# Optimization experiments

Hardware: AMD Instinct MI355X
Metric: run time of the kernel (lower is better)

Reference implementation:

```python
import jax, jax.numpy as jnp
import numpy as np

DT = 1.0          # integration timestep (ms)
SIGMA = 0.5       # gauss_std for surrogate (unused in pure fwd spike)
AMPLITUDE = 0.3   # dampening_factor
N = 50000         # neurons
R = 4             # receptor types
D = 5             # max_delay
E = 5000000       # recurrent synapses
B = 4             # batch


def setup_inputs() -> dict:
    key = jax.random.key(0)
    ks = jax.random.split(key, 20)
    f = jnp.float32
    inputs = jax.random.normal(ks[0], (B, N * R), f) * 0.1
    # z_buf holds binary spikes for the last D steps
    z_buf = jax.random.bernoulli(ks[1], 0.05, (B, N * D)).astype(f)
    v = jax.random.uniform(ks[2], (B, N), f, 0.0, 1.0)
    r = jnp.zeros((B, N), f)
    asc_1 = jax.random.normal(ks[3], (B, N), f)
    asc_2 = jax.random.normal(ks[4], (B, N), f)
    psc_rise = jax.random.normal(ks[5], (B, N * R), f) * 0.5
    psc = jax.random.normal(ks[6], (B, N * R), f)
    rec_w = jax.random.normal(ks[7], (E,), f) * 0.01
    rec_rows = jax.random.randint(ks[8], (E,), 0, N * R, jnp.int32)
    rec_cols = jax.random.randint(ks[9], (E,), 0, N * D, jnp.int32)
    syn_decay = jax.random.uniform(ks[10], (N, R), f, 0.5, 0.99)
    psc_initial = jax.random.uniform(ks[11], (N, R), f, 0.1, 1.0)
    t_ref = jax.random.uniform(ks[12], (N,), f, 1.0, 4.0)
    asc_amps = jax.random.normal(ks[13], (N, 2), f)
    k = jax.random.normal(ks[14], (N, 2), f)  # inv-sigmoid space, read via sigmoid
    v_th = jnp.ones((N,), f)
    e_l = jnp.zeros((N,), f)
    v_reset = jnp.zeros((N,), f)
    g = jax.random.uniform(ks[15], (N,), f, 0.1, 1.0)
    decay = jax.random.uniform(ks[16], (N,), f, 0.8, 0.99)
    current_factor = jax.random.uniform(ks[17], (N,), f, 0.1, 1.0)
    voltage_scale = jnp.ones((N,), f) * 20.0
    voltage_offset = jnp.ones((N,), f) * -70.0
    return dict(inputs=inputs, z_buf=z_buf, v=v, r=r, asc_1=asc_1, asc_2=asc_2,
                psc_rise=psc_rise, psc=psc, rec_w=rec_w, rec_rows=rec_rows,
                rec_cols=rec_cols, syn_decay=syn_decay, psc_initial=psc_initial,
                t_ref=t_ref, asc_amps=asc_amps, k=k, v_th=v_th, e_l=e_l,
                v_reset=v_reset, g=g, decay=decay, current_factor=current_factor,
                voltage_scale=voltage_scale, voltage_offset=voltage_offset)


def _step(inputs, z_buf, v, r, asc_1, asc_2, psc_rise, psc,
          rec_w, rec_rows, rec_cols, syn_decay, psc_initial, t_ref,
          asc_amps, k, v_th, e_l, v_reset, g, decay, current_factor,
          voltage_scale, voltage_offset):
    shaped_z_buf = z_buf.reshape(B, D, N)
    prev_z = shaped_z_buf[:, 0]                      # most recent spikes [B,N]
    psc_rise_r = psc_rise.reshape(B, N, R)
    psc_r = psc.reshape(B, N, R)

    # sparse recurrent matmul: W[N*R, N*D] @ z_buf^T -> [N*R, B]
    vals = rec_w[:, None] * z_buf.T[rec_cols]        # [E, B] gather
    i_rec = jax.ops.segment_sum(vals, rec_rows, num_segments=N * R).T  # [B, N*R]

    rec_inputs = (i_rec + inputs).reshape(B, N, R)
    new_psc_rise = syn_decay * psc_rise_r + rec_inputs * psc_initial
    new_psc = psc_r * syn_decay + DT * syn_decay * psc_rise_r

    new_r = jax.nn.relu(r + prev_z * t_ref - DT)

    kk = jax.nn.sigmoid(k)                           # param_k_read()
    new_asc_1 = jnp.exp(-DT * kk[:, 0]) * asc_1 + prev_z * asc_amps[:, 0]
    new_asc_2 = jnp.exp(-DT * kk[:, 1]) * asc_2 + prev_z * asc_amps[:, 1]

    reset_current = prev_z * (v_reset - v_th)
    input_current = psc_r.sum(-1)                    # old psc
    c1 = input_current + asc_1 + asc_2 + g * e_l
    new_v = decay * v + current_factor * c1 + reset_current

    v_sc = (new_v - v_th) / (v_th - e_l)
    new_z = (v_sc > 0.0).astype(v_sc.dtype)          # spike_gauss forward
    new_z = jnp.where(new_r > 0.0, jnp.zeros_like(new_z), new_z)

    new_z_buf = jnp.concatenate([new_z[:, None], shaped_z_buf[:, :-1]], axis=1)
    out_v = new_v * voltage_scale + voltage_offset
    return (new_z, out_v, new_r, new_asc_1, new_asc_2,
            new_psc_rise.reshape(B, N * R), new_psc.reshape(B, N * R),
            new_z_buf.reshape(B, N * D))


def reference(inputs, z_buf, v, r, asc_1, asc_2, psc_rise, psc,
              rec_w, rec_rows, rec_cols, syn_decay, psc_initial, t_ref,
              asc_amps, k, v_th, e_l, v_reset, g, decay, current_factor,
              voltage_scale, voltage_offset):
    outs = _step(inputs, z_buf, v, r, asc_1, asc_2, psc_rise, psc,
                 rec_w, rec_rows, rec_cols, syn_decay, psc_initial, t_ref,
                 asc_amps, k, v_th, e_l, v_reset, g, decay, current_factor,
                 voltage_scale, voltage_offset)
    # pack outputs + new state into one [B, N*(5+2R+D)] array
    return jnp.concatenate(outs, axis=-1)
```

## Files before the change

### kernel.cpp

```cpp
#include <hip/hip_runtime.h>

#define Nn 50000
#define Rr 4
#define Dd 5
#define Ee 5000000
#define Bb 4
#define NRr (Nn * Rr)
#define NDd (Nn * Dd)

__global__ void pack_z_kernel(const float* __restrict__ z_buf,
                              unsigned char* __restrict__ z_pack) {
    int i = blockIdx.x * blockDim.x + threadIdx.x;
    if (i >= NDd) return;
    unsigned m = 0;
#pragma unroll
    for (int b = 0; b < Bb; ++b)
        if (z_buf[(size_t)b * NDd + i] != 0.0f) m |= (1u << b);
    z_pack[i] = (unsigned char)m;
}

__global__ __launch_bounds__(256) void edge_kernel(
    const float4* __restrict__ w4, const int4* __restrict__ rows4,
    const int4* __restrict__ cols4, const unsigned char* __restrict__ z_pack,
    float* __restrict__ i_rec) {
    int i = blockIdx.x * blockDim.x + threadIdx.x;
    if (i >= Ee / 4) return;
    int4 c = cols4[i];
    int4 rw = rows4[i];
    float4 w = w4[i];
    unsigned m0 = z_pack[c.x];
    unsigned m1 = z_pack[c.y];
    unsigned m2 = z_pack[c.z];
    unsigned m3 = z_pack[c.w];
    if ((m0 | m1 | m2 | m3) == 0) return;
#define DO_EDGE(mm, row, wv)                                          \
    if (mm) {                                                         \
        if ((mm) & 1u) atomicAdd(&i_rec[0 * NRr + (row)], (wv));      \
        if ((mm) & 2u) atomicAdd(&i_rec[1 * NRr + (row)], (wv));      \
        if ((mm) & 4u) atomicAdd(&i_rec[2 * NRr + (row)], (wv));      \
        if ((mm) & 8u) atomicAdd(&i_rec[3 * NRr + (row)], (wv));      \
    }
    DO_EDGE(m0, rw.x, w.x)
    DO_EDGE(m1, rw.y, w.y)
    DO_EDGE(m2, rw.z, w.z)
    DO_EDGE(m3, rw.w, w.w)
#undef DO_EDGE
}

__global__ __launch_bounds__(256) void neuron_kernel(
    const float* __restrict__ inputs, const float* __restrict__ z_buf,
    const float* __restrict__ v_in, const float* __restrict__ r_in,
    const float* __restrict__ asc1_in, const float* __restrict__ asc2_in,
    const float* __restrict__ psc_rise_in, const float* __restrict__ psc_in,
    const float* __restrict__ syn_decay, const float* __restrict__ psc_initial,
    const float* __restrict__ t_ref, const float* __restrict__ asc_amps,
    const float* __restrict__ kparam, const float* __restrict__ v_th,
    const float* __restrict__ e_l, const float* __restrict__ v_reset,
    const float* __restrict__ g, const float* __restrict__ decay,
    const float* __restrict__ current_factor,
    const float* __restrict__ voltage_scale,
    const float* __restrict__ voltage_offset,
    const float* __restrict__ i_rec, float* __restrict__ out) {
    int n = blockIdx.x * blockDim.x + threadIdx.x;
    int b = blockIdx.y;
    if (n >= Nn) return;

    const size_t bn  = (size_t)b * Nn + n;
    const size_t bnr = (size_t)b * NRr + (size_t)n * 4;

    float prev_z = z_buf[(size_t)b * NDd + n];

    float4 ir  = *(const float4*)(i_rec + bnr);
    float4 in4 = *(const float4*)(inputs + bnr);
    float4 pr  = *(const float4*)(psc_rise_in + bnr);
    float4 pc  = *(const float4*)(psc_in + bnr);
    float4 sd  = *(const float4*)(syn_decay + (size_t)n * 4);
    float4 pi  = *(const float4*)(psc_initial + (size_t)n * 4);

    float4 npr, npc;
    npr.x = sd.x * pr.x + (ir.x + in4.x) * pi.x;
    npr.y = sd.y * pr.y + (ir.y + in4.y) * pi.y;
    npr.z = sd.z * pr.z + (ir.z + in4.z) * pi.z;
    npr.w = sd.w * pr.w + (ir.w + in4.w) * pi.w;
    npc.x = pc.x * sd.x + sd.x * pr.x;
    npc.y = pc.y * sd.y + sd.y * pr.y;
    npc.z = pc.z * sd.z + sd.z * pr.z;
    npc.w = pc.w * sd.w + sd.w * pr.w;

    float input_current = pc.x + pc.y + pc.z + pc.w;

    float tr    = t_ref[n];
    float new_r = fmaxf(r_in[bn] + prev_z * tr - 1.0f, 0.0f);

    float2 kv = *(const float2*)(kparam + (size_t)n * 2);
    float2 aa = *(const float2*)(asc_amps + (size_t)n * 2);
    float kk0 = 1.0f / (1.0f + expf(-kv.x));
    float kk1 = 1.0f / (1.0f + expf(-kv.y));
    float a1 = asc1_in[bn];
    float a2 = asc2_in[bn];
    float na1 = expf(-kk0) * a1 + prev_z * aa.x;
    float na2 = expf(-kk1) * a2 + prev_z * aa.y;

    float vth = v_th[n];
    float el  = e_l[n];
    float reset_current = prev_z * (v_reset[n] - vth);
    float c1 = input_current + a1 + a2 + g[n] * el;
    float new_v = decay[n] * v_in[bn] + current_factor[n] * c1 + reset_current;

    float v_sc = (new_v - vth) / (vth - el);
    float new_z = (v_sc > 0.0f) ? 1.0f : 0.0f;
    if (new_r > 0.0f) new_z = 0.0f;

    float out_v = new_v * voltage_scale[n] + voltage_offset[n];

    float* ob = out + (size_t)b * 18 * Nn;
    ob[n]            = new_z;
    ob[Nn + n]       = out_v;
    ob[2 * Nn + n]   = new_r;
    ob[3 * Nn + n]   = na1;
    ob[4 * Nn + n]   = na2;
    *(float4*)(ob + 5 * Nn + (size_t)n * 4) = npr;
    *(float4*)(ob + 9 * Nn + (size_t)n * 4) = npc;
    ob[13 * Nn + n] = new_z;
#pragma unroll
    for (int d = 0; d < Dd - 1; ++d)
        ob[14 * Nn + (size_t)d * Nn + n] = z_buf[(size_t)b * NDd + (size_t)d * Nn + n];
}

extern "C" void kernel_launch(void* const* d_in, const int* in_sizes, int n_in,
                              void* d_out, int out_size, void* d_ws, size_t ws_size,
                              hipStream_t stream) {
    const float* inputs        = (const float*)d_in[0];
    const float* z_buf         = (const float*)d_in[1];
    const float* v             = (const float*)d_in[2];
    const float* r             = (const float*)d_in[3];
    const float* asc_1         = (const float*)d_in[4];
    const float* asc_2         = (const float*)d_in[5];
    const float* psc_rise      = (const float*)d_in[6];
    const float* psc           = (const float*)d_in[7];
    const float* rec_w         = (const float*)d_in[8];
    const int*   rec_rows      = (const int*)d_in[9];
    const int*   rec_cols      = (const int*)d_in[10];
    const float* syn_decay     = (const float*)d_in[11];
    const float* psc_initial   = (const float*)d_in[12];
    const float* t_ref         = (const float*)d_in[13];
    const float* asc_amps      = (const float*)d_in[14];
    const float* k             = (const float*)d_in[15];
    const float* v_th          = (const float*)d_in[16];
    const float* e_l           = (const float*)d_in[17];
    const float* v_reset       = (const float*)d_in[18];
    const float* g             = (const float*)d_in[19];
    const float* decay         = (const float*)d_in[20];
    const float* current_factor= (const float*)d_in[21];
    const float* voltage_scale = (const float*)d_in[22];
    const float* voltage_offset= (const float*)d_in[23];
    float* out = (float*)d_out;

    float* i_rec = (float*)d_ws;
    unsigned char* z_pack = (unsigned char*)d_ws + (size_t)Bb * NRr * sizeof(float);

    hipMemsetAsync(i_rec, 0, (size_t)Bb * NRr * sizeof(float), stream);

    pack_z_kernel<<<(NDd + 255) / 256, 256, 0, stream>>>(z_buf, z_pack);

    edge_kernel<<<(Ee / 4 + 255) / 256, 256, 0, stream>>>(
        (const float4*)rec_w, (const int4*)rec_rows, (const int4*)rec_cols,
        z_pack, i_rec);

    dim3 ngrid((Nn + 255) / 256, Bb);
    neuron_kernel<<<ngrid, 256, 0, stream>>>(
        inputs, z_buf, v, r, asc_1, asc_2, psc_rise, psc,
        syn_decay, psc_initial, t_ref, asc_amps, k, v_th, e_l, v_reset,
        g, decay, current_factor, voltage_scale, voltage_offset,
        i_rec, out);
}
```

Before: 208.3 us.

## Use shared-memory spike bitmask to skip edge loads and fuse memset into pack

The pack kernel now also emits a one-bit-per-presynaptic-slot bitmask via wavefront ballot and zeroes the i_rec accumulator, which replaces the separate memset. The edge kernel is turned into a grid-stride loop over 2048 blocks. Each block loads the roughly 31KB bitmask into LDS, tests columns against it, and only fetches rows, weights and the per-batch byte mask for quads that contain an active column. This aims to avoid most rows/weights global reads and the random byte gathers, at the cost of a per-block LDS fill and lower occupancy from the large shared allocation.

Result: no change. 204.8 us (-1.7%).

```diff
diff --git a/kernel.cpp b/kernel.cpp
--- a/kernel.cpp
+++ b/kernel.cpp
@@ -7,44 +7,59 @@
 #define Bb 4
 #define NRr (Nn * Rr)
 #define NDd (Nn * Dd)
+#define ZW 7814
 
-__global__ void pack_z_kernel(const float* __restrict__ z_buf,
-                              unsigned char* __restrict__ z_pack) {
-    int i = blockIdx.x * blockDim.x + threadIdx.x;
-    if (i >= NDd) return;
+__global__ __launch_bounds__(256) void pack_z_kernel(
+    const float* __restrict__ z_buf, unsigned char* __restrict__ z_pack,
+    unsigned* __restrict__ zbits, float4* __restrict__ i_rec4) {
+    int i = blockIdx.x * 256 + threadIdx.x;
+    if (i < Bb * NRr / 4) i_rec4[i] = make_float4(0.f, 0.f, 0.f, 0.f);
     unsigned m = 0;
+    if (i < NDd) {
 #pragma unroll
-    for (int b = 0; b < Bb; ++b)
-        if (z_buf[(size_t)b * NDd + i] != 0.0f) m |= (1u << b);
-    z_pack[i] = (unsigned char)m;
+        for (int b = 0; b < Bb; ++b)
+            if (z_buf[(size_t)b * NDd + i] != 0.0f) m |= (1u << b);
+        z_pack[i] = (unsigned char)m;
+    }
+    unsigned long long bal = __ballot(m != 0);
+    if ((i & 63) == 0 && i < NDd) {
+        zbits[(i >> 5)]     = (unsigned)bal;
+        zbits[(i >> 5) + 1] = (unsigned)(bal >> 32);
+    }
 }
 
 __global__ __launch_bounds__(256) void edge_kernel(
     const float4* __restrict__ w4, const int4* __restrict__ rows4,
     const int4* __restrict__ cols4, const unsigned char* __restrict__ z_pack,
-    float* __restrict__ i_rec) {
-    int i = blockIdx.x * blockDim.x + threadIdx.x;
-    if (i >= Ee / 4) return;
-    int4 c = cols4[i];
-    int4 rw = rows4[i];
-    float4 w = w4[i];
-    unsigned m0 = z_pack[c.x];
-    unsigned m1 = z_pack[c.y];
-    unsigned m2 = z_pack[c.z];
-    unsigned m3 = z_pack[c.w];
-    if ((m0 | m1 | m2 | m3) == 0) return;
-#define DO_EDGE(mm, row, wv)                                          \
-    if (mm) {                                                         \
-        if ((mm) & 1u) atomicAdd(&i_rec[0 * NRr + (row)], (wv));      \
-        if ((mm) & 2u) atomicAdd(&i_rec[1 * NRr + (row)], (wv));      \
-        if ((mm) & 4u) atomicAdd(&i_rec[2 * NRr + (row)], (wv));      \
-        if ((mm) & 8u) atomicAdd(&i_rec[3 * NRr + (row)], (wv));      \
+    const unsigned* __restrict__ zbits, float* __restrict__ i_rec) {
+    __shared__ unsigned zb[ZW];
+    for (int t = threadIdx.x; t < ZW; t += 256) zb[t] = zbits[t];
+    __syncthreads();
+    const int nq = Ee / 4;
+    for (int i = blockIdx.x * 256 + threadIdx.x; i < nq;
+         i += gridDim.x * 256) {
+        int4 c = cols4[i];
+        unsigned h0 = (zb[(unsigned)c.x >> 5] >> (c.x & 31)) & 1u;
+        unsigned h1 = (zb[(unsigned)c.y >> 5] >> (c.y & 31)) & 1u;
+        unsigned h2 = (zb[(unsigned)c.z >> 5] >> (c.z & 31)) & 1u;
+        unsigned h3 = (zb[(unsigned)c.w >> 5] >> (c.w & 31)) & 1u;
+        if (!(h0 | h1 | h2 | h3)) continue;
+        int4 rw = rows4[i];
+        float4 w = w4[i];
+#define DO_EDGE(hh, col, row, wv)                                     \
+    if (hh) {                                                         \
+        unsigned mm = z_pack[col];                                    \
+        if (mm & 1u) atomicAdd(&i_rec[0 * NRr + (row)], (wv));        \
+        if (mm & 2u) atomicAdd(&i_rec[1 * NRr + (row)], (wv));        \
+        if (mm & 4u) atomicAdd(&i_rec[2 * NRr + (row)], (wv));        \
+        if (mm & 8u) atomicAdd(&i_rec[3 * NRr + (row)], (wv));        \
     }
-    DO_EDGE(m0, rw.x, w.x)
-    DO_EDGE(m1, rw.y, w.y)
-    DO_EDGE(m2, rw.z, w.z)
-    DO_EDGE(m3, rw.w, w.w)
+        DO_EDGE(h0, c.x, rw.x, w.x)
+        DO_EDGE(h1, c.y, rw.y, w.y)
+        DO_EDGE(h2, c.z, rw.z, w.z)
+        DO_EDGE(h3, c.w, rw.w, w.w)
 #undef DO_EDGE
+    }
 }
 
 __global__ __launch_bounds__(256) void neuron_kernel(
@@ -158,14 +173,14 @@
 
     float* i_rec = (float*)d_ws;
     unsigned char* z_pack = (unsigned char*)d_ws + (size_t)Bb * NRr * sizeof(float);
+    unsigned* zbits = (unsigned*)(z_pack + ((NDd + 255) & ~255));
 
-    hipMemsetAsync(i_rec, 0, (size_t)Bb * NRr * sizeof(float), stream);
+    pack_z_kernel<<<(NDd + 255) / 256, 256, 0, stream>>>(
+        z_buf, z_pack, zbits, (float4*)i_rec);
 
-    pack_z_kernel<<<(NDd + 255) / 256, 256, 0, stream>>>(z_buf, z_pack);
-
-    edge_kernel<<<(Ee / 4 + 255) / 256, 256, 0, stream>>>(
+    edge_kernel<<<2048, 256, 0, stream>>>(
         (const float4*)rec_w, (const int4*)rec_rows, (const int4*)rec_cols,
-        z_pack, i_rec);
+        z_pack, zbits, i_rec);
 
     dim3 ngrid((Nn + 255) / 256, Bb);
     neuron_kernel<<<ngrid, 256, 0, stream>>>(
```

## Fuse memset, pack, edge scatter and neuron update into one cooperative kernel

Applied to the files above, without the earlier changes.

Replaces the memset plus three kernel launches with a single cooperative kernel of 1024 blocks. It zeroes the accumulator, packs spikes, scatters edges and updates neurons in grid-strided phases separated by grid syncs. The edge phase now loads rows and weights only when some spike mask is nonzero, and uses nontemporal loads for the edge streams. This is meant to cut launch overhead and skip unneeded row and weight traffic. The cost is fewer resident threads for latency hiding and two grid-wide barriers, with a fallback to three ordinary kernels if the cooperative launch fails.

After: 493.8 us. 2.37x slower.

```diff
diff --git a/kernel.cpp b/kernel.cpp
--- a/kernel.cpp
+++ b/kernel.cpp
@@ -1,4 +1,7 @@
 #include <hip/hip_runtime.h>
+#include <hip/hip_cooperative_groups.h>
+
+namespace cg = cooperative_groups;
 
 #define Nn 50000
 #define Rr 4
@@ -8,169 +11,185 @@
 #define NRr (Nn * Rr)
 #define NDd (Nn * Dd)
 
-__global__ void pack_z_kernel(const float* __restrict__ z_buf,
-                              unsigned char* __restrict__ z_pack) {
-    int i = blockIdx.x * blockDim.x + threadIdx.x;
-    if (i >= NDd) return;
-    unsigned m = 0;
+typedef int   v4i __attribute__((ext_vector_type(4)));
+typedef float v4f __attribute__((ext_vector_type(4)));
+
+struct P {
+    const float* inputs; const float* z_buf; const float* v; const float* r;
+    const float* asc1; const float* asc2; const float* psc_rise; const float* psc;
+    const float* rec_w; const int* rec_rows; const int* rec_cols;
+    const float* syn_decay; const float* psc_initial; const float* t_ref;
+    const float* asc_amps; const float* k; const float* v_th; const float* e_l;
+    const float* v_reset; const float* g; const float* decay;
+    const float* current_factor; const float* vscale; const float* voffset;
+    float* out; float* i_rec; unsigned char* z_pack;
+};
+
+__device__ __forceinline__ void phase1_body(const P& p, int tid, int nthreads) {
+    for (int i = tid; i < Bb * NRr / 4; i += nthreads)
+        ((float4*)p.i_rec)[i] = make_float4(0.f, 0.f, 0.f, 0.f);
+    for (int i = tid; i < NDd; i += nthreads) {
+        unsigned m = 0;
 #pragma unroll
-    for (int b = 0; b < Bb; ++b)
-        if (z_buf[(size_t)b * NDd + i] != 0.0f) m |= (1u << b);
-    z_pack[i] = (unsigned char)m;
+        for (int b = 0; b < Bb; ++b)
+            if (p.z_buf[(size_t)b * NDd + i] != 0.0f) m |= (1u << b);
+        p.z_pack[i] = (unsigned char)m;
+    }
 }
 
-__global__ __launch_bounds__(256) void edge_kernel(
-    const float4* __restrict__ w4, const int4* __restrict__ rows4,
-    const int4* __restrict__ cols4, const unsigned char* __restrict__ z_pack,
-    float* __restrict__ i_rec) {
-    int i = blockIdx.x * blockDim.x + threadIdx.x;
-    if (i >= Ee / 4) return;
-    int4 c = cols4[i];
-    int4 rw = rows4[i];
-    float4 w = w4[i];
-    unsigned m0 = z_pack[c.x];
-    unsigned m1 = z_pack[c.y];
-    unsigned m2 = z_pack[c.z];
-    unsigned m3 = z_pack[c.w];
-    if ((m0 | m1 | m2 | m3) == 0) return;
-#define DO_EDGE(mm, row, wv)                                          \
-    if (mm) {                                                         \
-        if ((mm) & 1u) atomicAdd(&i_rec[0 * NRr + (row)], (wv));      \
-        if ((mm) & 2u) atomicAdd(&i_rec[1 * NRr + (row)], (wv));      \
-        if ((mm) & 4u) atomicAdd(&i_rec[2 * NRr + (row)], (wv));      \
-        if ((mm) & 8u) atomicAdd(&i_rec[3 * NRr + (row)], (wv));      \
+__device__ __forceinline__ void phase2_body(const P& p, int tid, int nthreads) {
+    const v4i* cols4 = (const v4i*)p.rec_cols;
+    const v4i* rows4 = (const v4i*)p.rec_rows;
+    const v4f* w4    = (const v4f*)p.rec_w;
+    const unsigned char* zp = p.z_pack;
+    float* i_rec = p.i_rec;
+    for (int i = tid; i < Ee / 4; i += nthreads) {
+        v4i c = __builtin_nontemporal_load(&cols4[i]);
+        unsigned m0 = zp[c.x], m1 = zp[c.y], m2 = zp[c.z], m3 = zp[c.w];
+        if (!(m0 | m1 | m2 | m3)) continue;
+        v4i rw = __builtin_nontemporal_load(&rows4[i]);
+        v4f w  = __builtin_nontemporal_load(&w4[i]);
+        auto do_edge = [&](unsigned mm, int row, float wv) {
+            if (mm & 1u) atomicAdd(&i_rec[0 * NRr + row], wv);
+            if (mm & 2u) atomicAdd(&i_rec[1 * NRr + row], wv);
+            if (mm & 4u) atomicAdd(&i_rec[2 * NRr + row], wv);
+            if (mm & 8u) atomicAdd(&i_rec[3 * NRr + row], wv);
+        };
+        do_edge(m0, rw.x, w.x);
+        do_edge(m1, rw.y, w.y);
+        do_edge(m2, rw.z, w.z);
+        do_edge(m3, rw.w, w.w);
     }
-    DO_EDGE(m0, rw.x, w.x)
-    DO_EDGE(m1, rw.y, w.y)
-    DO_EDGE(m2, rw.z, w.z)
-    DO_EDGE(m3, rw.w, w.w)
-#undef DO_EDGE
 }
 
-__global__ __launch_bounds__(256) void neuron_kernel(
-    const float* __restrict__ inputs, const float* __restrict__ z_buf,
-    const float* __restrict__ v_in, const float* __restrict__ r_in,
-    const float* __restrict__ asc1_in, const float* __restrict__ asc2_in,
-    const float* __restrict__ psc_rise_in, const float* __restrict__ psc_in,
-    const float* __restrict__ syn_decay, const float* __restrict__ psc_initial,
-    const float* __restrict__ t_ref, const float* __restrict__ asc_amps,
-    const float* __restrict__ kparam, const float* __restrict__ v_th,
-    const float* __restrict__ e_l, const float* __restrict__ v_reset,
-    const float* __restrict__ g, const float* __restrict__ decay,
-    const float* __restrict__ current_factor,
-    const float* __restrict__ voltage_scale,
-    const float* __restrict__ voltage_offset,
-    const float* __restrict__ i_rec, float* __restrict__ out) {
-    int n = blockIdx.x * blockDim.x + threadIdx.x;
-    int b = blockIdx.y;
-    if (n >= Nn) return;
+__device__ __forceinline__ void phase3_body(const P& p, int tid, int nthreads) {
+    for (int idx = tid; idx < Bb * Nn; idx += nthreads) {
+        int b = idx / Nn;
+        int n = idx - b * Nn;
+        const size_t bn  = (size_t)b * Nn + n;
+        const size_t bnr = (size_t)b * NRr + (size_t)n * 4;
 
-    const size_t bn  = (size_t)b * Nn + n;
-    const size_t bnr = (size_t)b * NRr + (size_t)n * 4;
+        float prev_z = p.z_buf[(size_t)b * NDd + n];
 
-    float prev_z = z_buf[(size_t)b * NDd + n];
+        float4 ir  = *(const float4*)(p.i_rec + bnr);
+        float4 in4 = *(const float4*)(p.inputs + bnr);
+        float4 pr  = *(const float4*)(p.psc_rise + bnr);
+        float4 pc  = *(const float4*)(p.psc + bnr);
+        float4 sd  = *(const float4*)(p.syn_decay + (size_t)n * 4);
+        float4 pi  = *(const float4*)(p.psc_initial + (size_t)n * 4);
 
-    float4 ir  = *(const float4*)(i_rec + bnr);
-    float4 in4 = *(const float4*)(inputs + bnr);
-    float4 pr  = *(const float4*)(psc_rise_in + bnr);
-    float4 pc  = *(const float4*)(psc_in + bnr);
-    float4 sd  = *(const float4*)(syn_decay + (size_t)n * 4);
-    float4 pi  = *(const float4*)(psc_initial + (size_t)n * 4);
+        float4 npr, npc;
+        npr.x = sd.x * pr.x + (ir.x + in4.x) * pi.x;
+        npr.y = sd.y * pr.y + (ir.y + in4.y) * pi.y;
+        npr.z = sd.z * pr.z + (ir.z + in4.z) * pi.z;
+        npr.w = sd.w * pr.w + (ir.w + in4.w) * pi.w;
+        npc.x = pc.x * sd.x + sd.x * pr.x;
+        npc.y = pc.y * sd.y + sd.y * pr.y;
+        npc.z = pc.z * sd.z + sd.z * pr.z;
+        npc.w = pc.w * sd.w + sd.w * pr.w;
 
-    float4 npr, npc;
-    npr.x = sd.x * pr.x + (ir.x + in4.x) * pi.x;
-    npr.y = sd.y * pr.y + (ir.y + in4.y) * pi.y;
-    npr.z = sd.z * pr.z + (ir.z + in4.z) * pi.z;
-    npr.w = sd.w * pr.w + (ir.w + in4.w) * pi.w;
-    npc.x = pc.x * sd.x + sd.x * pr.x;
-    npc.y = pc.y * sd.y + sd.y * pr.y;
-    npc.z = pc.z * sd.z + sd.z * pr.z;
-    npc.w = pc.w * sd.w + sd.w * pr.w;
+        float input_current = pc.x + pc.y + pc.z + pc.w;
 
-    float input_current = pc.x + pc.y + pc.z + pc.w;
+        float tr    = p.t_ref[n];
+        float new_r = fmaxf(p.r[bn] + prev_z * tr - 1.0f, 0.0f);
 
-    float tr    = t_ref[n];
-    float new_r = fmaxf(r_in[bn] + prev_z * tr - 1.0f, 0.0f);
+        float2 kv = *(const float2*)(p.k + (size_t)n * 2);
+        float2 aa = *(const float2*)(p.asc_amps + (size_t)n * 2);
+        float kk0 = 1.0f / (1.0f + expf(-kv.x));
+        float kk1 = 1.0f / (1.0f + expf(-kv.y));
+        float a1 = p.asc1[bn];
+        float a2 = p.asc2[bn];
+        float na1 = expf(-kk0) * a1 + prev_z * aa.x;
+        float na2 = expf(-kk1) * a2 + prev_z * aa.y;
 
-    float2 kv = *(const float2*)(kparam + (size_t)n * 2);
-    float2 aa = *(const float2*)(asc_amps + (size_t)n * 2);
-    float kk0 = 1.0f / (1.0f + expf(-kv.x));
-    float kk1 = 1.0f / (1.0f + expf(-kv.y));
-    float a1 = asc1_in[bn];
-    float a2 = asc2_in[bn];
-    float na1 = expf(-kk0) * a1 + prev_z * aa.x;
-    float na2 = expf(-kk1) * a2 + prev_z * aa.y;
+        float vth = p.v_th[n];
+        float el  = p.e_l[n];
+        float reset_current = prev_z * (p.v_reset[n] - vth);
+        float c1 = input_current + a1 + a2 + p.g[n] * el;
+        float new_v = p.decay[n] * p.v[bn] + p.current_factor[n] * c1 + reset_current;
 
-    float vth = v_th[n];
-    float el  = e_l[n];
-    float reset_current = prev_z * (v_reset[n] - vth);
-    float c1 = input_current + a1 + a2 + g[n] * el;
-    float new_v = decay[n] * v_in[bn] + current_factor[n] * c1 + reset_current;
+        float v_sc = (new_v - vth) / (vth - el);
+        float new_z = (v_sc > 0.0f) ? 1.0f : 0.0f;
+        if (new_r > 0.0f) new_z = 0.0f;
 
-    float v_sc = (new_v - vth) / (vth - el);
-    float new_z = (v_sc > 0.0f) ? 1.0f : 0.0f;
-    if (new_r > 0.0f) new_z = 0.0f;
+        float out_v = new_v * p.vscale[n] + p.voffset[n];
 
-    float out_v = new_v * voltage_scale[n] + voltage_offset[n];
+        float* ob = p.out + (size_t)b * 18 * Nn;
+        ob[n]            = new_z;
+        ob[Nn + n]       = out_v;
+        ob[2 * Nn + n]   = new_r;
+        ob[3 * Nn + n]   = na1;
+        ob[4 * Nn + n]   = na2;
+        *(float4*)(ob + 5 * Nn + (size_t)n * 4) = npr;
+        *(float4*)(ob + 9 * Nn + (size_t)n * 4) = npc;
+        ob[13 * Nn + n] = new_z;
+#pragma unroll
+        for (int d = 0; d < Dd - 1; ++d)
+            ob[14 * Nn + (size_t)d * Nn + n] =
+                p.z_buf[(size_t)b * NDd + (size_t)d * Nn + n];
+    }
+}
 
-    float* ob = out + (size_t)b * 18 * Nn;
-    ob[n]            = new_z;
-    ob[Nn + n]       = out_v;
-    ob[2 * Nn + n]   = new_r;
-    ob[3 * Nn + n]   = na1;
-    ob[4 * Nn + n]   = na2;
-    *(float4*)(ob + 5 * Nn + (size_t)n * 4) = npr;
-    *(float4*)(ob + 9 * Nn + (size_t)n * 4) = npc;
-    ob[13 * Nn + n] = new_z;
-#pragma unroll
-    for (int d = 0; d < Dd - 1; ++d)
-        ob[14 * Nn + (size_t)d * Nn + n] = z_buf[(size_t)b * NDd + (size_t)d * Nn + n];
+__global__ __launch_bounds__(256, 4) void fused_kernel(P p) {
+    cg::grid_group grid = cg::this_grid();
+    const int tid = blockIdx.x * 256 + threadIdx.x;
+    const int nthreads = gridDim.x * 256;
+    phase1_body(p, tid, nthreads);
+    grid.sync();
+    phase2_body(p, tid, nthreads);
+    grid.sync();
+    phase3_body(p, tid, nthreads);
+}
+
+__global__ __launch_bounds__(256) void phase1_kernel(P p) {
+    phase1_body(p, blockIdx.x * 256 + threadIdx.x, gridDim.x * 256);
+}
+__global__ __launch_bounds__(256) void phase2_kernel(P p) {
+    phase2_body(p, blockIdx.x * 256 + threadIdx.x, gridDim.x * 256);
+}
+__global__ __launch_bounds__(256) void phase3_kernel(P p) {
+    phase3_body(p, blockIdx.x * 256 + threadIdx.x, gridDim.x * 256);
 }
 
 extern "C" void kernel_launch(void* const* d_in, const int* in_sizes, int n_in,
                               void* d_out, int out_size, void* d_ws, size_t ws_size,
                               hipStream_t stream) {
-    const float* inputs        = (const float*)d_in[0];
-    const float* z_buf         = (const float*)d_in[1];
-    const float* v             = (const float*)d_in[2];
-    const float* r             = (const float*)d_in[3];
-    const float* asc_1         = (const float*)d_in[4];
-    const float* asc_2         = (const float*)d_in[5];
-    const float* psc_rise      = (const float*)d_in[6];
-    const float* psc           = (const float*)d_in[7];
-    const float* rec_w         = (const float*)d_in[8];
-    const int*   rec_rows      = (const int*)d_in[9];
-    const int*   rec_cols      = (const int*)d_in[10];
-    const float* syn_decay     = (const float*)d_in[11];
-    const float* psc_initial   = (const float*)d_in[12];
-    const float* t_ref         = (const float*)d_in[13];
-    const float* asc_amps      = (const float*)d_in[14];
-    const float* k             = (const float*)d_in[15];
-    const float* v_th          = (const float*)d_in[16];
-    const float* e_l           = (const float*)d_in[17];
-    const float* v_reset       = (const float*)d_in[18];
-    const float* g             = (const float*)d_in[19];
-    const float* decay         = (const float*)d_in[20];
-    const float* current_factor= (const float*)d_in[21];
-    const float* voltage_scale = (const float*)d_in[22];
-    const float* voltage_offset= (const float*)d_in[23];
-    float* out = (float*)d_out;
+    P p;
+    p.inputs        = (const float*)d_in[0];
+    p.z_buf         = (const float*)d_in[1];
+    p.v             = (const float*)d_in[2];
+    p.r             = (const float*)d_in[3];
+    p.asc1          = (const float*)d_in[4];
+    p.asc2          = (const float*)d_in[5];
+    p.psc_rise      = (const float*)d_in[6];
+    p.psc           = (const float*)d_in[7];
+    p.rec_w         = (const float*)d_in[8];
+    p.rec_rows      = (const int*)d_in[9];
+    p.rec_cols      = (const int*)d_in[10];
+    p.syn_decay     = (const float*)d_in[11];
+    p.psc_initial   = (const float*)d_in[12];
+    p.t_ref         = (const float*)d_in[13];
+    p.asc_amps      = (const float*)d_in[14];
+    p.k             = (const float*)d_in[15];
+    p.v_th          = (const float*)d_in[16];
+    p.e_l           = (const float*)d_in[17];
+    p.v_reset       = (const float*)d_in[18];
+    p.g             = (const float*)d_in[19];
+    p.decay         = (const float*)d_in[20];
+    p.current_factor= (const float*)d_in[21];
+    p.vscale        = (const float*)d_in[22];
+    p.voffset       = (const float*)d_in[23];
+    p.out           = (float*)d_out;
+    p.i_rec  = (float*)d_ws;
+    p.z_pack = (unsigned char*)d_ws + 3200000;
 
-    float* i_rec = (float*)d_ws;
-    unsigned char* z_pack = (unsigned char*)d_ws + (size_t)Bb * NRr * sizeof(float);
-
-    hipMemsetAsync(i_rec, 0, (size_t)Bb * NRr * sizeof(float), stream);
-
-    pack_z_kernel<<<(NDd + 255) / 256, 256, 0, stream>>>(z_buf, z_pack);
-
-    edge_kernel<<<(Ee / 4 + 255) / 256, 256, 0, stream>>>(
-        (const float4*)rec_w, (const int4*)rec_rows, (const int4*)rec_cols,
-        z_pack, i_rec);
-
-    dim3 ngrid((Nn + 255) / 256, Bb);
-    neuron_kernel<<<ngrid, 256, 0, stream>>>(
-        inputs, z_buf, v, r, asc_1, asc_2, psc_rise, psc,
-        syn_decay, psc_initial, t_ref, asc_amps, k, v_th, e_l, v_reset,
-        g, decay, current_factor, voltage_scale, voltage_offset,
-        i_rec, out);
+    void* args[] = {(void*)&p};
+    hipError_t err = hipLaunchCooperativeKernel(
+        reinterpret_cast<void*>(fused_kernel), dim3(1024), dim3(256),
+        args, 0, stream);
+    if (err != hipSuccess) {
+        phase1_kernel<<<(NDd + 255) / 256, 256, 0, stream>>>(p);
+        phase2_kernel<<<(Ee / 4 + 255) / 256, 256, 0, stream>>>(p);
+        phase3_kernel<<<(Bb * Nn + 255) / 256, 256, 0, stream>>>(p);
+    }
 }
```
